# Kernel tuning notes

Hardware: AMD Instinct MI355X
Metric: run time of the kernel (lower is better)

The kernel has to match this reference:

```python
import jax, jax.numpy as jnp
import numpy as np

NEG_INF = -1.0e10  # matches -10000000000.0 in the original


def setup_inputs() -> dict:
    key0 = jax.random.key(0)
    kq, kk, kv = jax.random.split(key0, 3)
    b, t, n, n_kv, d = 1, 2048, 32, 8, 128
    query = jax.random.normal(kq, (b, t, n, d), dtype=jnp.float32)
    key = jax.random.normal(kk, (b, t, n_kv, d), dtype=jnp.float32)
    value = jax.random.normal(kv, (b, t, n_kv, d), dtype=jnp.float32)
    return {"query": query, "key": key, "value": value}


def reference(query, key, value):
    """PagedAttentionOp prefill path: paged_dot_product_attention_with_max_and_sum.

    Returns (attn, local_max, local_sums) exactly as the flax module does.
    """
    b, t, n, d = query.shape
    _, s, n_kv, _ = key.shape
    g = n // n_kv  # query heads per KV head (GQA group size)
    q = jnp.reshape(query, (b, t, n_kv, g, d))
    # [b, n_kv, g, t, s]
    attn_weights = jnp.einsum("btkgd,bskd->bkgts", q, key)
    causal_mask = jnp.triu(jnp.ones((t, s), dtype=bool), k=1)[None, None, None]
    masked = jnp.where(causal_mask, NEG_INF, attn_weights)
    local_max = jnp.max(masked, axis=-1, keepdims=True)          # [b,k,g,t,1]
    local_exps = jnp.exp(masked - local_max)
    local_sums = jnp.sum(local_exps, axis=-1, keepdims=True)     # [b,k,g,t,1]
    attn = jnp.einsum("bkgts,bskd->btkgd", local_exps, value)
    attn = jnp.reshape(attn, (b, t, n, d))
    # move the t axis to position 1 then flatten (k,g) -> n
    local_max = jnp.reshape(jnp.moveaxis(local_max, -2, 1), (b, t, n, 1))
    local_sums = jnp.reshape(jnp.moveaxis(local_sums, -2, 1), (b, t, n, 1))
    return attn, local_max, local_sums
```

## Files before the change

### kernel.cpp

```cpp
#include <hip/hip_runtime.h>
#include <hip/hip_bf16.h>

#define TT  2048
#define NH  32
#define NKV 8
#define DD  128
#define KVB 64
#define THR 8.0f

typedef __attribute__((ext_vector_type(8)))  short  short8;
typedef __attribute__((ext_vector_type(4)))  float  f32x4;
typedef __attribute__((ext_vector_type(16))) float  f32x16;
typedef unsigned int u32;
typedef __attribute__((ext_vector_type(4)))  u32    u32x4;

static __device__ __forceinline__ short f2bf(float x) {
  __bf16 b = (__bf16)x;
  return __builtin_bit_cast(short, b);
}
static __device__ __forceinline__ short8 cvt8(f32x4 a, f32x4 b) {
  short8 r;
  r[0]=f2bf(a[0]); r[1]=f2bf(a[1]); r[2]=f2bf(a[2]); r[3]=f2bf(a[3]);
  r[4]=f2bf(b[0]); r[5]=f2bf(b[1]); r[6]=f2bf(b[2]); r[7]=f2bf(b[3]);
  return r;
}
static __device__ __forceinline__ u32 pk2(float lo, float hi) {
  const u32 a = (u32)(unsigned short)f2bf(lo);
  const u32 b = (u32)(unsigned short)f2bf(hi);
  return a | (b << 16);
}
static __device__ __forceinline__ void gload_lds16(const short* g, short* l) {
  __builtin_amdgcn_global_load_lds(
      (const __attribute__((address_space(1))) u32*)g,
      (__attribute__((address_space(3))) u32*)l, 16, 0, 0);
}

__global__ __launch_bounds__(256) void preconv(
    const float* __restrict__ K, const float* __restrict__ V,
    short* __restrict__ Kbf, short* __restrict__ Vtbf)
{
  const int t = threadIdx.x;
  if (blockIdx.x >= 256) {
    const int b  = blockIdx.x - 256;
    const int rr = (b << 6) + (t >> 2);
    const int q  = t & 3;
    const int j = rr >> 3, kvh = rr & 7;
    const float* src = K + (size_t)rr * DD + q * 32;
    short* dst = Kbf + ((size_t)kvh * TT + j) * DD + q * 32;
#pragma unroll
    for (int i = 0; i < 4; ++i) {
      f32x4 a  = *reinterpret_cast<const f32x4*>(src + i * 8);
      f32x4 bb = *reinterpret_cast<const f32x4*>(src + i * 8 + 4);
      *reinterpret_cast<short8*>(dst + i * 8) = cvt8(a, bb);
    }
  } else {
    const int kvh = blockIdx.x >> 5, jt = blockIdx.x & 31;
    __shared__ short Vl[64][136];
    const int jl = t >> 2, q = t & 3;
    const float* src = V + ((size_t)(jt * 64 + jl) * NKV + kvh) * DD + q * 32;
#pragma unroll
    for (int i = 0; i < 4; ++i) {
      f32x4 a  = *reinterpret_cast<const f32x4*>(src + i * 8);
      f32x4 bb = *reinterpret_cast<const f32x4*>(src + i * 8 + 4);
      *reinterpret_cast<short8*>(&Vl[jl][q * 32 + i * 8]) = cvt8(a, bb);
    }
    __syncthreads();
    const int d = t >> 1, jh = t & 1;
    short8 o[4];
#pragma unroll
    for (int k = 0; k < 4; ++k)
#pragma unroll
      for (int i = 0; i < 8; ++i)
        o[k][i] = Vl[jh * 32 + k * 8 + i][d];
    short* dst = Vtbf + ((size_t)kvh * DD + d) * TT + jt * 64 + jh * 32;
#pragma unroll
    for (int k = 0; k < 4; ++k)
      *reinterpret_cast<short8*>(dst + k * 8) = o[k];
  }
}

__global__ __launch_bounds__(512, 2) void attn_fwd(
    const float* __restrict__ Q, const short* __restrict__ Kbf,
    const short* __restrict__ Vtbf, float* __restrict__ O,
    float* __restrict__ Mo, float* __restrict__ Lo)
{
  __shared__ __align__(16) short smem[2*KVB*DD + 2*DD*KVB];
  __shared__ float sx[3][2][4][32];

  short (*Kb)[KVB][DD] = reinterpret_cast<short(*)[KVB][DD]>(&smem[0]);
  short (*Vt)[DD][KVB] = reinterpret_cast<short(*)[DD][KVB]>(&smem[2*KVB*DD]);

  const int bid  = blockIdx.x;
  const int kvh  = bid & (NKV - 1);
  const int q32  = 63 - (bid >> 3);
  const int wv   = threadIdx.x >> 6;
  const int headq= wv & 3;
  const int kh   = wv >> 2;
  const int lane = threadIdx.x & 63;
  const int l31  = lane & 31;
  const int hiK  = lane >> 5;
  const int l7   = lane & 7;
  const int head = kvh * 4 + headq;
  const int qbase = q32 * 32;
  const int q    = qbase + l31;

  const int krow0 = 8 * wv + (lane >> 4);
  const int koff0 = krow0 * DD + ((lane & 15) ^ (krow0 & 7)) * 8;
  const int krow1 = krow0 + 4;
  const int koff1 = krow1 * DD + ((lane & 15) ^ (krow1 & 7)) * 8;
  const int vrow0 = 16 * wv + (lane >> 3);
  const int voff0 = vrow0 * TT + ((lane & 7) ^ (lane >> 3)) * 8;
  const int voff1 = voff0 + 8 * TT;

  short8 aq[8];
  {
    const float* qp = Q + ((size_t)q * NH + head) * DD + hiK * 8;
#pragma unroll
    for (int ks = 0; ks < 8; ++ks) {
      const float* p = qp + ks * 16;
      aq[ks] = cvt8(*reinterpret_cast<const f32x4*>(p),
                    *reinterpret_cast<const f32x4*>(p + 4));
    }
  }

  f32x16 acc[4];
#pragma unroll
  for (int i = 0; i < 4; ++i) acc[i] = (f32x16)0.0f;
  float m = -INFINITY, tmaxh = -INFINITY, lsum = 0.0f;

  const int ntiles = (q32 >> 1) + 1;

  const short* kgp = Kbf + (size_t)kvh * TT * DD;
  const short* vgp = Vtbf + (size_t)kvh * DD * TT;

  gload_lds16(kgp + koff0, &Kb[0][8 * wv][0]);
  gload_lds16(kgp + koff1, &Kb[0][8 * wv + 4][0]);
  gload_lds16(vgp + voff0, &Vt[0][16 * wv][0]);
  gload_lds16(vgp + voff1, &Vt[0][16 * wv + 8][0]);
  kgp += (size_t)KVB * DD;
  vgp += KVB;

  for (int jt = 0; jt < ntiles; ++jt) {
    const int j0  = jt << 6;
    const int buf = jt & 1;

    __syncthreads();

    f32x16 st = (f32x16)0.0f;
    const short* kr = &Kb[buf][kh * 32 + l31][0];
    __builtin_amdgcn_s_setprio(1);
#pragma unroll
    for (int ks = 0; ks < 8; ++ks) {
      const int c = ((ks << 1) | hiK) ^ l7;
      short8 kb = *reinterpret_cast<const short8*>(kr + c * 8);
      st = __builtin_amdgcn_mfma_f32_32x32x16_bf16(kb, aq[ks], st, 0, 0, 0);
    }
    __builtin_amdgcn_s_setprio(0);

    if (jt + 1 < ntiles) {
      const int nb = buf ^ 1;
      gload_lds16(kgp + koff0, &Kb[nb][8 * wv][0]);
      gload_lds16(kgp + koff1, &Kb[nb][8 * wv + 4][0]);
      gload_lds16(vgp + voff0, &Vt[nb][16 * wv][0]);
      gload_lds16(vgp + voff1, &Vt[nb][16 * wv + 8][0]);
      kgp += (size_t)KVB * DD;
      vgp += KVB;
    }

    if (jt == ntiles - 1) {
#pragma unroll
      for (int r = 0; r < 16; ++r) {
        const int key = j0 + kh * 32 + (r & 3) + 8 * (r >> 2) + 4 * hiK;
        if (key > q) st[r] = -1.0e10f;
      }
    }

    float mx = st[0];
#pragma unroll
    for (int r = 1; r < 16; ++r) mx = fmaxf(mx, st[r]);
    mx = fmaxf(mx, __shfl_xor(mx, 32, 64));
    tmaxh = fmaxf(tmaxh, mx);

    if (__any(mx > m + THR)) {
      const float mn = fmaxf(m, mx);
      const float sc = __expf(m - mn);
      m = mn;
      lsum *= sc;
#pragma unroll
      for (int r = 0; r < 16; ++r) {
        const float sf = __shfl(sc, (r & 3) + 8 * (r >> 2) + 4 * hiK, 64);
        acc[0][r] *= sf; acc[1][r] *= sf; acc[2][r] *= sf; acc[3][r] *= sf;
      }
    }

    float e[16];
#pragma unroll
    for (int r = 0; r < 16; ++r) e[r] = __expf(st[r] - m);
    lsum += (((e[0]+e[1])+(e[2]+e[3]))+((e[4]+e[5])+(e[6]+e[7])))
          + (((e[8]+e[9])+(e[10]+e[11]))+((e[12]+e[13])+(e[14]+e[15])));

    short8 pa[2];
#pragma unroll
    for (int h2 = 0; h2 < 2; ++h2) {
      const int b = 8 * h2;
      u32 u0 = pk2(e[b+0], e[b+1]);
      u32 u1 = pk2(e[b+2], e[b+3]);
      u32 u2 = pk2(e[b+4], e[b+5]);
      u32 u3 = pk2(e[b+6], e[b+7]);
      u32 sA = hiK ? u0 : u2;
      u32 sB = hiK ? u1 : u3;
      u32 rA = __shfl_xor(sA, 32, 64);
      u32 rB = __shfl_xor(sB, 32, 64);
      u32x4 w;
      w[0] = hiK ? rA : u0;
      w[1] = hiK ? rB : u1;
      w[2] = hiK ? u2 : rA;
      w[3] = hiK ? u3 : rB;
      pa[h2] = __builtin_bit_cast(short8, w);
    }

    __builtin_amdgcn_s_setprio(1);
#pragma unroll
    for (int dg = 0; dg < 4; ++dg) {
      const short* vr = &Vt[buf][dg * 32 + l31][0];
#pragma unroll
      for (int h2 = 0; h2 < 2; ++h2) {
        const int ksv = 2 * kh + h2;
        const int c = ((ksv << 1) | hiK) ^ l7;
        short8 vb = *reinterpret_cast<const short8*>(vr + c * 8);
        acc[dg] = __builtin_amdgcn_mfma_f32_32x32x16_bf16(pa[h2], vb, acc[dg], 0, 0, 0);
      }
    }
    __builtin_amdgcn_s_setprio(0);
  }

  const float lw = lsum + __shfl_xor(lsum, 32, 64);
  __syncthreads();
  if (lane < 32) {
    sx[0][kh][headq][lane] = m;
    sx[1][kh][headq][lane] = tmaxh;
    sx[2][kh][headq][lane] = lw;
  }
  __syncthreads();
  const float mo   = sx[0][kh ^ 1][headq][l31];
  const float to   = sx[1][kh ^ 1][headq][l31];
  const float lo2  = sx[2][kh ^ 1][headq][l31];
  const float tmax = fmaxf(tmaxh, to);
  const float fsA  = __expf(m - tmax);
  const float ltot = lw * fsA + lo2 * __expf(mo - tmax);

  float* mbuf = reinterpret_cast<float*>(&smem[0]);
  if (kh == 1) {
#pragma unroll
    for (int r = 0; r < 16; ++r) {
      const int row = (r & 3) + 8 * (r >> 2) + 4 * hiK;
      const float sfr = __shfl(fsA, row, 64);
#pragma unroll
      for (int dg = 0; dg < 4; ++dg)
        mbuf[headq * 4096 + row * 128 + dg * 32 + l31] = acc[dg][r] * sfr;
    }
  }
  __syncthreads();
  if (kh == 0) {
#pragma unroll
    for (int r = 0; r < 16; ++r) {
      const int row = (r & 3) + 8 * (r >> 2) + 4 * hiK;
      const float sfr = __shfl(fsA, row, 64);
      const size_t ob = ((size_t)(qbase + row) * NH + head) * DD + l31;
#pragma unroll
      for (int dg = 0; dg < 4; ++dg)
        O[ob + dg * 32] = acc[dg][r] * sfr + mbuf[headq * 4096 + row * 128 + dg * 32 + l31];
    }
    if (lane < 32) {
      Mo[(size_t)q * NH + head] = tmax;
      Lo[(size_t)q * NH + head] = ltot;
    }
  }
}

extern "C" void kernel_launch(void* const* d_in, const int* in_sizes, int n_in,
                              void* d_out, int out_size, void* d_ws, size_t ws_size,
                              hipStream_t stream) {
  const float* Q = (const float*)d_in[0];
  const float* K = (const float*)d_in[1];
  const float* V = (const float*)d_in[2];
  float* O  = (float*)d_out;
  float* Mo = O + (size_t)TT * NH * DD;
  float* Lo = Mo + (size_t)TT * NH;
  short* Kbf  = (short*)d_ws;
  short* Vtbf = Kbf + (size_t)NKV * TT * DD;
  preconv<<<dim3(512), dim3(256), 0, stream>>>(K, V, Kbf, Vtbf);
  attn_fwd<<<dim3(64 * NKV), dim3(512), 0, stream>>>(Q, Kbf, Vtbf, O, Mo, Lo);
}
```

Before: 81.44 us.

## Split KV tile across three wave groups with 96-key tiles

Grows the KV tile from 64 to 96 keys and the block from 8 to 12 waves, so three groups of four waves each take a 32-key slice. Each tile now has more parallel work and the causal loop runs fewer iterations. The prefetch of the next tile moves ahead of the QK MFMAs, and the V staging is rewritten to use a 128-wide row buffer with bounds clamping. The final merge becomes a three-way reduction through shared memory with an extra barrier. Larger LDS use and register pressure at 768 threads may lower occupancy, and the last tile may include keys that are only masked out.

```diff
diff --git a/kernel.cpp b/kernel.cpp
--- a/kernel.cpp
+++ b/kernel.cpp
@@ -5,7 +5,8 @@
 #define NH  32
 #define NKV 8
 #define DD  128
-#define KVB 64
+#define KVB 96
+#define VROW 128
 #define THR 8.0f
 
 typedef __attribute__((ext_vector_type(8)))  short  short8;
@@ -79,23 +80,23 @@
   }
 }
 
-__global__ __launch_bounds__(512, 2) void attn_fwd(
+__global__ __launch_bounds__(768, 3) void attn_fwd(
     const float* __restrict__ Q, const short* __restrict__ Kbf,
     const short* __restrict__ Vtbf, float* __restrict__ O,
     float* __restrict__ Mo, float* __restrict__ Lo)
 {
-  __shared__ __align__(16) short smem[2*KVB*DD + 2*DD*KVB];
-  __shared__ float sx[3][2][4][32];
-
-  short (*Kb)[KVB][DD] = reinterpret_cast<short(*)[KVB][DD]>(&smem[0]);
-  short (*Vt)[DD][KVB] = reinterpret_cast<short(*)[DD][KVB]>(&smem[2*KVB*DD]);
+  __shared__ __align__(16) short smem[2*KVB*DD + 2*DD*VROW];
+  __shared__ float sx[3][3][4][32];
+
+  short (*Kb)[KVB][DD]   = reinterpret_cast<short(*)[KVB][DD]>(&smem[0]);
+  short (*Vt)[DD][VROW]  = reinterpret_cast<short(*)[DD][VROW]>(&smem[2*KVB*DD]);
 
   const int bid  = blockIdx.x;
   const int kvh  = bid & (NKV - 1);
   const int q32  = 63 - (bid >> 3);
   const int wv   = threadIdx.x >> 6;
   const int headq= wv & 3;
-  const int kh   = wv >> 2;
+  const int ks3  = wv >> 2;
   const int lane = threadIdx.x & 63;
   const int l31  = lane & 31;
   const int hiK  = lane >> 5;
@@ -104,13 +105,24 @@
   const int qbase = q32 * 32;
   const int q    = qbase + l31;
 
-  const int krow0 = 8 * wv + (lane >> 4);
-  const int koff0 = krow0 * DD + ((lane & 15) ^ (krow0 & 7)) * 8;
-  const int krow1 = krow0 + 4;
-  const int koff1 = krow1 * DD + ((lane & 15) ^ (krow1 & 7)) * 8;
-  const int vrow0 = 16 * wv + (lane >> 3);
-  const int voff0 = vrow0 * TT + ((lane & 7) ^ (lane >> 3)) * 8;
-  const int voff1 = voff0 + 8 * TT;
+  const int krw0  = 8 * wv + (lane >> 4);
+  const int koff0 = krw0 * DD + ((lane & 15) ^ (krw0 & 7)) * 8;
+  const int krw1  = krw0 + 4;
+  const int koff1 = krw1 * DD + ((lane & 15) ^ (krw1 & 7)) * 8;
+  int voffA[3], vkeyA[3];
+  const int nvw = (wv < 8) ? 3 : 2;
+#pragma unroll
+  for (int t = 0; t < 3; ++t) {
+    const int w   = (wv + 12 * t) & 31;
+    const int row = 4 * w + (lane >> 4);
+    int c = (lane & 15) ^ (row & 7);
+    if (c >= 12) c = 0;
+    voffA[t] = row * TT + 8 * c;
+    vkeyA[t] = 8 * c;
+  }
+
+  const short* kB = Kbf + (size_t)kvh * TT * DD;
+  const short* vB = Vtbf + (size_t)kvh * DD * TT;
 
   short8 aq[8];
   {
@@ -128,26 +140,32 @@
   for (int i = 0; i < 4; ++i) acc[i] = (f32x16)0.0f;
   float m = -INFINITY, tmaxh = -INFINITY, lsum = 0.0f;
 
-  const int ntiles = (q32 >> 1) + 1;
-
-  const short* kgp = Kbf + (size_t)kvh * TT * DD;
-  const short* vgp = Vtbf + (size_t)kvh * DD * TT;
-
-  gload_lds16(kgp + koff0, &Kb[0][8 * wv][0]);
-  gload_lds16(kgp + koff1, &Kb[0][8 * wv + 4][0]);
-  gload_lds16(vgp + voff0, &Vt[0][16 * wv][0]);
-  gload_lds16(vgp + voff1, &Vt[0][16 * wv + 8][0]);
-  kgp += (size_t)KVB * DD;
-  vgp += KVB;
+  const int ntiles = (q32 + 3) / 3;
+
+  auto STAGE = [&](int bn, int jt2) {
+    const int jk = 96 * jt2;
+    const short* kS = kB + (size_t)jk * DD;
+    const short* vS = vB + jk;
+    gload_lds16(((jk + krw0 < TT) ? kS : kB) + koff0, &Kb[bn][8 * wv][0]);
+    gload_lds16(((jk + krw1 < TT) ? kS : kB) + koff1, &Kb[bn][8 * wv + 4][0]);
+    short* vd = &Vt[bn][0][0];
+    gload_lds16(((jk + vkeyA[0] < TT) ? vS : vB) + voffA[0], vd + wv * 512);
+    gload_lds16(((jk + vkeyA[1] < TT) ? vS : vB) + voffA[1], vd + (wv + 12) * 512);
+    if (nvw == 3)
+      gload_lds16(((jk + vkeyA[2] < TT) ? vS : vB) + voffA[2], vd + (wv + 24) * 512);
+  };
+
+  STAGE(0, 0);
 
   for (int jt = 0; jt < ntiles; ++jt) {
-    const int j0  = jt << 6;
     const int buf = jt & 1;
 
     __syncthreads();
 
+    if (jt + 1 < ntiles) STAGE(buf ^ 1, jt + 1);
+
     f32x16 st = (f32x16)0.0f;
-    const short* kr = &Kb[buf][kh * 32 + l31][0];
+    const short* kr = &Kb[buf][ks3 * 32 + l31][0];
     __builtin_amdgcn_s_setprio(1);
 #pragma unroll
     for (int ks = 0; ks < 8; ++ks) {
@@ -157,20 +175,10 @@
     }
     __builtin_amdgcn_s_setprio(0);
 
-    if (jt + 1 < ntiles) {
-      const int nb = buf ^ 1;
-      gload_lds16(kgp + koff0, &Kb[nb][8 * wv][0]);
-      gload_lds16(kgp + koff1, &Kb[nb][8 * wv + 4][0]);
-      gload_lds16(vgp + voff0, &Vt[nb][16 * wv][0]);
-      gload_lds16(vgp + voff1, &Vt[nb][16 * wv + 8][0]);
-      kgp += (size_t)KVB * DD;
-      vgp += KVB;
-    }
-
     if (jt == ntiles - 1) {
 #pragma unroll
       for (int r = 0; r < 16; ++r) {
-        const int key = j0 + kh * 32 + (r & 3) + 8 * (r >> 2) + 4 * hiK;
+        const int key = 96 * jt + 32 * ks3 + (r & 3) + 8 * (r >> 2) + 4 * hiK;
         if (key > q) st[r] = -1.0e10f;
       }
     }
@@ -211,12 +219,12 @@
       u32 sB = hiK ? u1 : u3;
       u32 rA = __shfl_xor(sA, 32, 64);
       u32 rB = __shfl_xor(sB, 32, 64);
-      u32x4 w;
-      w[0] = hiK ? rA : u0;
-      w[1] = hiK ? rB : u1;
-      w[2] = hiK ? u2 : rA;
-      w[3] = hiK ? u3 : rB;
-      pa[h2] = __builtin_bit_cast(short8, w);
+      u32x4 w4;
+      w4[0] = hiK ? rA : u0;
+      w4[1] = hiK ? rB : u1;
+      w4[2] = hiK ? u2 : rA;
+      w4[3] = hiK ? u3 : rB;
+      pa[h2] = __builtin_bit_cast(short8, w4);
     }
 
     __builtin_amdgcn_s_setprio(1);
@@ -225,7 +233,7 @@
       const short* vr = &Vt[buf][dg * 32 + l31][0];
 #pragma unroll
       for (int h2 = 0; h2 < 2; ++h2) {
-        const int ksv = 2 * kh + h2;
+        const int ksv = 2 * ks3 + h2;
         const int c = ((ksv << 1) | hiK) ^ l7;
         short8 vb = *reinterpret_cast<const short8*>(vr + c * 8);
         acc[dg] = __builtin_amdgcn_mfma_f32_32x32x16_bf16(pa[h2], vb, acc[dg], 0, 0, 0);
@@ -237,39 +245,52 @@
   const float lw = lsum + __shfl_xor(lsum, 32, 64);
   __syncthreads();
   if (lane < 32) {
-    sx[0][kh][headq][lane] = m;
-    sx[1][kh][headq][lane] = tmaxh;
-    sx[2][kh][headq][lane] = lw;
+    sx[0][ks3][headq][lane] = m;
+    sx[1][ks3][headq][lane] = tmaxh;
+    sx[2][ks3][headq][lane] = lw;
   }
   __syncthreads();
-  const float mo   = sx[0][kh ^ 1][headq][l31];
-  const float to   = sx[1][kh ^ 1][headq][l31];
-  const float lo2  = sx[2][kh ^ 1][headq][l31];
-  const float tmax = fmaxf(tmaxh, to);
-  const float fsA  = __expf(m - tmax);
-  const float ltot = lw * fsA + lo2 * __expf(mo - tmax);
+  const float m0 = sx[0][0][headq][l31], m1 = sx[0][1][headq][l31], m2 = sx[0][2][headq][l31];
+  const float t0 = sx[1][0][headq][l31], t1 = sx[1][1][headq][l31], t2 = sx[1][2][headq][l31];
+  const float l0 = sx[2][0][headq][l31], l1 = sx[2][1][headq][l31], l2 = sx[2][2][headq][l31];
+  const float tmax = fmaxf(fmaxf(t0, t1), t2);
+  const float fs   = __expf(m - tmax);
+  const float ltot = l0 * __expf(m0 - tmax) + l1 * __expf(m1 - tmax)
+                   + l2 * __expf(m2 - tmax);
 
   float* mbuf = reinterpret_cast<float*>(&smem[0]);
-  if (kh == 1) {
+  if (ks3 == 2) {
 #pragma unroll
     for (int r = 0; r < 16; ++r) {
       const int row = (r & 3) + 8 * (r >> 2) + 4 * hiK;
-      const float sfr = __shfl(fsA, row, 64);
+      const float sfr = __shfl(fs, row, 64);
 #pragma unroll
       for (int dg = 0; dg < 4; ++dg)
         mbuf[headq * 4096 + row * 128 + dg * 32 + l31] = acc[dg][r] * sfr;
     }
   }
   __syncthreads();
-  if (kh == 0) {
+  if (ks3 == 1) {
 #pragma unroll
     for (int r = 0; r < 16; ++r) {
       const int row = (r & 3) + 8 * (r >> 2) + 4 * hiK;
-      const float sfr = __shfl(fsA, row, 64);
+      const float sfr = __shfl(fs, row, 64);
+#pragma unroll
+      for (int dg = 0; dg < 4; ++dg)
+        mbuf[headq * 4096 + row * 128 + dg * 32 + l31] += acc[dg][r] * sfr;
+    }
+  }
+  __syncthreads();
+  if (ks3 == 0) {
+#pragma unroll
+    for (int r = 0; r < 16; ++r) {
+      const int row = (r & 3) + 8 * (r >> 2) + 4 * hiK;
+      const float sfr = __shfl(fs, row, 64);
       const size_t ob = ((size_t)(qbase + row) * NH + head) * DD + l31;
 #pragma unroll
       for (int dg = 0; dg < 4; ++dg)
-        O[ob + dg * 32] = acc[dg][r] * sfr + mbuf[headq * 4096 + row * 128 + dg * 32 + l31];
+        O[ob + dg * 32] = acc[dg][r] * sfr
+                        + mbuf[headq * 4096 + row * 128 + dg * 32 + l31];
     }
     if (lane < 32) {
       Mo[(size_t)q * NH + head] = tmax;
@@ -290,5 +311,5 @@
   short* Kbf  = (short*)d_ws;
   short* Vtbf = Kbf + (size_t)NKV * TT * DD;
   preconv<<<dim3(512), dim3(256), 0, stream>>>(K, V, Kbf, Vtbf);
-  attn_fwd<<<dim3(64 * NKV), dim3(512), 0, stream>>>(Q, Kbf, Vtbf, O, Mo, Lo);
-}
+  attn_fwd<<<dim3(64 * NKV), dim3(768), 0, stream>>>(Q, Kbf, Vtbf, O, Mo, Lo);
+}
```

Result: slower. 87.82 us (+7.8%).
